# Kernel optimization log

Measured on AMD Instinct MI355X. Metric: run time of the kernel, lower is better.

The kernel has to match this reference:

```python
import jax, jax.numpy as jnp
import numpy as np

N_NODES = 400000
NUM_GRAPHS = 2048
IN_FEAT = 256
DENSE = 128
N_HEADS = 8


def setup_inputs() -> dict:
    key = jax.random.key(0)
    k_h, k_seg, k_w1, k_b1, k_w2, k_b2 = jax.random.split(key, 6)
    h = jax.random.normal(k_h, (N_NODES, IN_FEAT), dtype=jnp.float32)
    segment_ids = jnp.sort(
        jax.random.randint(k_seg, (N_NODES,), 0, NUM_GRAPHS, dtype=jnp.int32))
    # Linear params (jax convention: x @ W + b)
    W1 = jax.random.normal(k_w1, (IN_FEAT, DENSE), dtype=jnp.float32) / np.sqrt(IN_FEAT)
    b1 = jax.random.normal(k_b1, (DENSE,), dtype=jnp.float32) * 0.01
    W2 = jax.random.normal(k_w2, (DENSE, N_HEADS), dtype=jnp.float32) / np.sqrt(DENSE)
    b2 = jax.random.normal(k_b2, (N_HEADS,), dtype=jnp.float32) * 0.01
    return {"h": h, "segment_ids": segment_ids, "W1": W1, "b1": b1,
            "W2": W2, "b2": b2, "num_graphs": NUM_GRAPHS}


def reference(h, segment_ids, W1, b1, W2, b2, num_graphs):
    # scores: fc2(tanh(fc1(h))) -> [N, n_heads]
    scores = jnp.tanh(h @ W1 + b1) @ W2 + b2
    # ragged (per-graph) softmax over nodes, per head (dgl.softmax_nodes)
    seg_max = jax.ops.segment_max(scores, segment_ids, num_segments=num_graphs)  # [G, H]
    ex = jnp.exp(scores - seg_max[segment_ids])                                  # [N, H]
    denom = jax.ops.segment_sum(ex, segment_ids, num_segments=num_graphs)        # [G, H]
    attn = ex / denom[segment_ids]                                               # [N, H]
    # mean over heads of per-head weighted segment sums == segment sum with
    # head-averaged weights (linearity), avoiding H separate ndata passes.
    w = attn.mean(axis=1)                                                         # [N]
    out = jax.ops.segment_sum(h * w[:, None], segment_ids, num_segments=num_graphs)  # [G, in_feat]
    return out
```

## Files before the change

kernel.cpp:

```cpp
#include <hip/hip_runtime.h>
#include <hip/hip_bf16.h>

#define IN_FEAT 256
#define DENSE   128
#define NHEADS  8
#define MAXN    384
#define LDA     264
#define LDT     132
#define LDW2    132

typedef __attribute__((ext_vector_type(8))) short bf16x8_t;
typedef __attribute__((ext_vector_type(4))) float f32x4_t;

__device__ __forceinline__ unsigned int f2bf(float f) {
  unsigned int u = __float_as_uint(f);
  u += 0x7fffu + ((u >> 16) & 1u);
  return u >> 16;
}

__device__ __forceinline__ float fast_tanh(float x) {
  float ax = fabsf(x);
  float e = __expf(-2.0f * ax);
  float t = (1.0f - e) / (1.0f + e);
  return copysignf(t, x);
}

__global__ void seg_offsets_kernel(const int* __restrict__ seg, int* __restrict__ offs,
                                   int N, int G) {
  int i = blockIdx.x * blockDim.x + threadIdx.x;
  if (i >= N) return;
  int s  = seg[i];
  int sp = (i == 0) ? -1 : seg[i - 1];
  for (int g = sp + 1; g <= s; ++g) offs[g] = i;
  if (i == N - 1) {
    for (int g = s + 1; g <= G; ++g) offs[g] = N;
  }
}

__device__ __forceinline__ int lower_bound_dev(const int* __restrict__ seg, int N, int v) {
  int lo = 0, hi = N;
  while (lo < hi) {
    int mid = (lo + hi) >> 1;
    if (seg[mid] < v) lo = mid + 1; else hi = mid;
  }
  return lo;
}

__launch_bounds__(256, 3)
__global__ void attn_pool_kernel(const float* __restrict__ h,
                                 const int* __restrict__ seg,
                                 const int* __restrict__ offs,
                                 const float* __restrict__ W1,
                                 const float* __restrict__ b1,
                                 const float* __restrict__ W2,
                                 const float* __restrict__ b2,
                                 float* __restrict__ out,
                                 int N) {
  __shared__ short sA[64 * LDA];
  __shared__ float sScores[MAXN * NHEADS];
  __shared__ float sWgt[MAXN];
  __shared__ float sW2T[NHEADS * LDW2];
  __shared__ float sB1[DENSE];
  __shared__ float sB2[NHEADS];
  __shared__ float sRed[64];
  __shared__ float sMax[NHEADS];
  __shared__ float sInvD[NHEADS];

  const int g   = blockIdx.x;
  const int tid = threadIdx.x;

  int start, end;
  if (offs != nullptr) {
    start = offs[g];
    end   = offs[g + 1];
  } else {
    start = lower_bound_dev(seg, N, g);
    end   = lower_bound_dev(seg, N, g + 1);
  }
  int n = end - start;
  if (n > MAXN) n = MAXN;

  float* sT = (float*)sA;

  if (n == 0) {
    if (tid < IN_FEAT) out[(size_t)g * IN_FEAT + tid] = 0.0f;
    return;
  }

  for (int idx = tid; idx < DENSE * NHEADS; idx += 256) {
    int k = idx >> 3; int hd = idx & 7;
    sW2T[hd * LDW2 + k] = W2[idx];
  }
  if (tid < DENSE)  sB1[tid] = b1[tid];
  if (tid < NHEADS) sB2[tid] = b2[tid];

  const int lane = tid & 63;
  const int wv   = tid >> 6;
  const int lr   = lane & 15;
  const int q    = lane >> 4;

  bf16x8_t b1f[16];
  #pragma unroll
  for (int ct = 0; ct < 2; ++ct) {
    int colb = wv * 32 + ct * 16 + lr;
    #pragma unroll
    for (int ks = 0; ks < 8; ++ks) {
      bf16x8_t bb;
      #pragma unroll
      for (int j = 0; j < 8; ++j) {
        float f = W1[(ks * 32 + q * 8 + j) * DENSE + colb];
        bb[j] = (short)f2bf(f);
      }
      b1f[ct * 8 + ks] = bb;
    }
  }

  const int ntiles = (n + 63) >> 6;
  for (int t = 0; t < ntiles; ++t) {
    const int m0   = start + t * 64;
    const int rem  = n - t * 64;
    const int mcnt = rem < 64 ? rem : 64;
    __syncthreads();

    #pragma unroll
    for (int it = 0; it < 16; ++it) {
      int row = it * 4 + (tid >> 6);
      int f4  = tid & 63;
      float4 v = make_float4(0.f, 0.f, 0.f, 0.f);
      if (row < mcnt) v = *(const float4*)(h + (size_t)(m0 + row) * IN_FEAT + f4 * 4);
      unsigned int p0 = f2bf(v.x) | (f2bf(v.y) << 16);
      unsigned int p1 = f2bf(v.z) | (f2bf(v.w) << 16);
      *(uint2*)&sA[row * LDA + f4 * 4] = make_uint2(p0, p1);
    }
    __syncthreads();

    f32x4_t acc[4][2];
    #pragma unroll
    for (int mt = 0; mt < 4; ++mt) {
      acc[mt][0] = (f32x4_t){0, 0, 0, 0};
      acc[mt][1] = (f32x4_t){0, 0, 0, 0};
    }
    #pragma unroll
    for (int ks = 0; ks < 8; ++ks) {
      bf16x8_t a0 = *(const bf16x8_t*)&sA[( 0 + lr) * LDA + ks * 32 + q * 8];
      bf16x8_t a1 = *(const bf16x8_t*)&sA[(16 + lr) * LDA + ks * 32 + q * 8];
      bf16x8_t a2 = *(const bf16x8_t*)&sA[(32 + lr) * LDA + ks * 32 + q * 8];
      bf16x8_t a3 = *(const bf16x8_t*)&sA[(48 + lr) * LDA + ks * 32 + q * 8];
      acc[0][0] = __builtin_amdgcn_mfma_f32_16x16x32_bf16(a0, b1f[ks],     acc[0][0], 0, 0, 0);
      acc[0][1] = __builtin_amdgcn_mfma_f32_16x16x32_bf16(a0, b1f[8 + ks], acc[0][1], 0, 0, 0);
      acc[1][0] = __builtin_amdgcn_mfma_f32_16x16x32_bf16(a1, b1f[ks],     acc[1][0], 0, 0, 0);
      acc[1][1] = __builtin_amdgcn_mfma_f32_16x16x32_bf16(a1, b1f[8 + ks], acc[1][1], 0, 0, 0);
      acc[2][0] = __builtin_amdgcn_mfma_f32_16x16x32_bf16(a2, b1f[ks],     acc[2][0], 0, 0, 0);
      acc[2][1] = __builtin_amdgcn_mfma_f32_16x16x32_bf16(a2, b1f[8 + ks], acc[2][1], 0, 0, 0);
      acc[3][0] = __builtin_amdgcn_mfma_f32_16x16x32_bf16(a3, b1f[ks],     acc[3][0], 0, 0, 0);
      acc[3][1] = __builtin_amdgcn_mfma_f32_16x16x32_bf16(a3, b1f[8 + ks], acc[3][1], 0, 0, 0);
    }
    __syncthreads();

    #pragma unroll
    for (int mt = 0; mt < 4; ++mt) {
      int rbase = mt * 16 + q * 4;
      #pragma unroll
      for (int ct = 0; ct < 2; ++ct) {
        int col = wv * 32 + ct * 16 + lr;
        float bias = sB1[col];
        #pragma unroll
        for (int r = 0; r < 4; ++r)
          sT[(rbase + r) * LDT + col] = fast_tanh(acc[mt][ct][r] + bias);
      }
    }
    __syncthreads();

    {
      int i0 = tid >> 3;
      int hd = tid & 7;
      #pragma unroll
      for (int half = 0; half < 2; ++half) {
        int i = i0 + half * 32;
        if (i < mcnt) {
          float s = sB2[hd];
          #pragma unroll
          for (int k4 = 0; k4 < DENSE; k4 += 4) {
            float4 tv  = *(const float4*)&sT[i * LDT + k4];
            float4 wv2 = *(const float4*)&sW2T[hd * LDW2 + k4];
            s = fmaf(tv.x, wv2.x, s); s = fmaf(tv.y, wv2.y, s);
            s = fmaf(tv.z, wv2.z, s); s = fmaf(tv.w, wv2.w, s);
          }
          sScores[(t * 64 + i) * NHEADS + hd] = s;
        }
      }
    }
  }
  __syncthreads();

  if (tid < 64) {
    int hd = tid & 7, ch = tid >> 3;
    float m = -3.4e38f;
    for (int i = ch; i < n; i += 8) m = fmaxf(m, sScores[i * NHEADS + hd]);
    sRed[tid] = m;
  }
  __syncthreads();
  if (tid < NHEADS) {
    float m = sRed[tid];
    #pragma unroll
    for (int j = 1; j < 8; ++j) m = fmaxf(m, sRed[j * 8 + tid]);
    sMax[tid] = m;
  }
  __syncthreads();
  if (tid < 64) {
    int hd = tid & 7, ch = tid >> 3;
    float mm = sMax[hd], ssum = 0.f;
    for (int i = ch; i < n; i += 8) {
      float e = __expf(sScores[i * NHEADS + hd] - mm);
      sScores[i * NHEADS + hd] = e;
      ssum += e;
    }
    sRed[tid] = ssum;
  }
  __syncthreads();
  if (tid < NHEADS) {
    float d = 0.f;
    #pragma unroll
    for (int j = 0; j < 8; ++j) d += sRed[j * 8 + tid];
    sInvD[tid] = 1.0f / d;
  }
  __syncthreads();
  for (int i = tid; i < n; i += 256) {
    float w = 0.f;
    #pragma unroll
    for (int hd = 0; hd < NHEADS; ++hd) w += sScores[i * NHEADS + hd] * sInvD[hd];
    sWgt[i] = 0.125f * w;
  }
  __syncthreads();

  {
    int grp = tid >> 6;
    int c4  = lane << 2;
    float4 acc = make_float4(0.f, 0.f, 0.f, 0.f);
    for (int i = grp; i < n; i += 4) {
      float w = sWgt[i];
      float4 hv = *(const float4*)(h + (size_t)(start + i) * IN_FEAT + c4);
      acc.x = fmaf(w, hv.x, acc.x);
      acc.y = fmaf(w, hv.y, acc.y);
      acc.z = fmaf(w, hv.z, acc.z);
      acc.w = fmaf(w, hv.w, acc.w);
    }
    float* sPart = (float*)sA;
    *(float4*)&sPart[grp * IN_FEAT + c4] = acc;
    __syncthreads();
    {
      float o = 0.f;
      #pragma unroll
      for (int p = 0; p < 4; ++p) o += sPart[p * IN_FEAT + tid];
      out[(size_t)g * IN_FEAT + tid] = o;
    }
  }
}

extern "C" void kernel_launch(void* const* d_in, const int* in_sizes, int n_in,
                              void* d_out, int out_size, void* d_ws, size_t ws_size,
                              hipStream_t stream) {
  const float* h   = (const float*)d_in[0];
  const int*   seg = (const int*)d_in[1];
  const float* W1  = (const float*)d_in[2];
  const float* b1v = (const float*)d_in[3];
  const float* W2  = (const float*)d_in[4];
  const float* b2v = (const float*)d_in[5];
  float* out = (float*)d_out;
  const int N = in_sizes[0] / IN_FEAT;
  const int G = out_size / IN_FEAT;

  int* offs = nullptr;
  if (ws_size >= (size_t)(G + 1) * sizeof(int)) {
    offs = (int*)d_ws;
    seg_offsets_kernel<<<(N + 255) / 256, 256, 0, stream>>>(seg, offs, N, G);
  }
  attn_pool_kernel<<<G, 256, 0, stream>>>(h, seg, offs, W1, b1v, W2, b2v, out, N);
}
```

Measured before the change: 237.5 us.

## Prefetch next h tile into registers and prepack W1 bf16 fragments

Adds a small kernel that converts W1 once into bf16 MFMA fragment order in the workspace, so the main kernel reads packed fragments each k-step instead of holding 16 converted fragments in registers. The main kernel also software-pipelines the h tile load: the next 64-row tile is issued into registers while the current tile runs its MFMAs. Tanh is applied in registers before the LDS store, and the softmax reductions now use all 256 threads instead of 64. The aim is to hide global load latency and cut per-block W1 conversion, at the cost of 64 prefetch registers, repeated W1 fragment reads from cache every tile, and one extra launch.

```diff
diff --git a/kernel.cpp b/kernel.cpp
--- a/kernel.cpp
+++ b/kernel.cpp
@@ -37,6 +37,27 @@
   }
 }
 
+__global__ void w1_frag_kernel(const float* __restrict__ W1, unsigned int* __restrict__ w1f) {
+  int t = blockIdx.x * blockDim.x + threadIdx.x;
+  if (t >= 4096) return;
+  int lane = t & 63;
+  int fid  = t >> 6;
+  int ct = fid & 1;
+  int ks = (fid >> 1) & 7;
+  int wv = fid >> 4;
+  int col = wv * 32 + ct * 16 + (lane & 15);
+  int k0  = ks * 32 + (lane >> 4) * 8;
+  unsigned int p[4];
+  #pragma unroll
+  for (int jj = 0; jj < 4; ++jj) {
+    unsigned int lo = f2bf(W1[(size_t)(k0 + 2 * jj) * DENSE + col]);
+    unsigned int hi = f2bf(W1[(size_t)(k0 + 2 * jj + 1) * DENSE + col]);
+    p[jj] = lo | (hi << 16);
+  }
+  uint4 v = make_uint4(p[0], p[1], p[2], p[3]);
+  *(uint4*)&w1f[(size_t)t * 4] = v;
+}
+
 __device__ __forceinline__ int lower_bound_dev(const int* __restrict__ seg, int N, int v) {
   int lo = 0, hi = N;
   while (lo < hi) {
@@ -51,6 +72,7 @@
                                  const int* __restrict__ seg,
                                  const int* __restrict__ offs,
                                  const float* __restrict__ W1,
+                                 const unsigned int* __restrict__ w1f,
                                  const float* __restrict__ b1,
                                  const float* __restrict__ W2,
                                  const float* __restrict__ b2,
@@ -62,7 +84,7 @@
   __shared__ float sW2T[NHEADS * LDW2];
   __shared__ float sB1[DENSE];
   __shared__ float sB2[NHEADS];
-  __shared__ float sRed[64];
+  __shared__ float sRed[256];
   __shared__ float sMax[NHEADS];
   __shared__ float sInvD[NHEADS];
 
@@ -87,35 +109,32 @@
     return;
   }
 
-  for (int idx = tid; idx < DENSE * NHEADS; idx += 256) {
-    int k = idx >> 3; int hd = idx & 7;
-    sW2T[hd * LDW2 + k] = W2[idx];
-  }
-  if (tid < DENSE)  sB1[tid] = b1[tid];
-  if (tid < NHEADS) sB2[tid] = b2[tid];
-
   const int lane = tid & 63;
   const int wv   = tid >> 6;
   const int lr   = lane & 15;
   const int q    = lane >> 4;
-
-  bf16x8_t b1f[16];
-  #pragma unroll
-  for (int ct = 0; ct < 2; ++ct) {
-    int colb = wv * 32 + ct * 16 + lr;
-    #pragma unroll
-    for (int ks = 0; ks < 8; ++ks) {
-      bf16x8_t bb;
-      #pragma unroll
-      for (int j = 0; j < 8; ++j) {
-        float f = W1[(ks * 32 + q * 8 + j) * DENSE + colb];
-        bb[j] = (short)f2bf(f);
-      }
-      b1f[ct * 8 + ks] = bb;
-    }
-  }
-
   const int ntiles = (n + 63) >> 6;
+
+  float4 pf[16];
+  const int pfr  = tid >> 6;
+  const int pfc4 = (tid & 63) * 4;
+  auto pf_issue = [&](int m0_) {
+    #pragma unroll
+    for (int it = 0; it < 16; ++it) {
+      int rr = m0_ + it * 4 + pfr;
+      rr = (rr < end) ? rr : start;
+      pf[it] = *(const float4*)(h + (size_t)rr * IN_FEAT + pfc4);
+    }
+  };
+  pf_issue(start);
+
+  for (int idx = tid; idx < DENSE * NHEADS; idx += 256) {
+    int k = idx >> 3; int hd = idx & 7;
+    sW2T[hd * LDW2 + k] = W2[idx];
+  }
+  if (tid < DENSE)  sB1[tid] = b1[tid];
+  if (tid < NHEADS) sB2[tid] = b2[tid];
+
   for (int t = 0; t < ntiles; ++t) {
     const int m0   = start + t * 64;
     const int rem  = n - t * 64;
@@ -124,15 +143,16 @@
 
     #pragma unroll
     for (int it = 0; it < 16; ++it) {
-      int row = it * 4 + (tid >> 6);
-      int f4  = tid & 63;
-      float4 v = make_float4(0.f, 0.f, 0.f, 0.f);
-      if (row < mcnt) v = *(const float4*)(h + (size_t)(m0 + row) * IN_FEAT + f4 * 4);
+      int row = it * 4 + pfr;
+      float4 v = pf[it];
+      if (row >= mcnt) v = make_float4(0.f, 0.f, 0.f, 0.f);
       unsigned int p0 = f2bf(v.x) | (f2bf(v.y) << 16);
       unsigned int p1 = f2bf(v.z) | (f2bf(v.w) << 16);
-      *(uint2*)&sA[row * LDA + f4 * 4] = make_uint2(p0, p1);
-    }
-    __syncthreads();
+      *(uint2*)&sA[row * LDA + pfc4] = make_uint2(p0, p1);
+    }
+    __syncthreads();
+
+    if (t + 1 < ntiles) pf_issue(m0 + 64);
 
     f32x4_t acc[4][2];
     #pragma unroll
@@ -140,21 +160,56 @@
       acc[mt][0] = (f32x4_t){0, 0, 0, 0};
       acc[mt][1] = (f32x4_t){0, 0, 0, 0};
     }
-    #pragma unroll
-    for (int ks = 0; ks < 8; ++ks) {
-      bf16x8_t a0 = *(const bf16x8_t*)&sA[( 0 + lr) * LDA + ks * 32 + q * 8];
-      bf16x8_t a1 = *(const bf16x8_t*)&sA[(16 + lr) * LDA + ks * 32 + q * 8];
-      bf16x8_t a2 = *(const bf16x8_t*)&sA[(32 + lr) * LDA + ks * 32 + q * 8];
-      bf16x8_t a3 = *(const bf16x8_t*)&sA[(48 + lr) * LDA + ks * 32 + q * 8];
-      acc[0][0] = __builtin_amdgcn_mfma_f32_16x16x32_bf16(a0, b1f[ks],     acc[0][0], 0, 0, 0);
-      acc[0][1] = __builtin_amdgcn_mfma_f32_16x16x32_bf16(a0, b1f[8 + ks], acc[0][1], 0, 0, 0);
-      acc[1][0] = __builtin_amdgcn_mfma_f32_16x16x32_bf16(a1, b1f[ks],     acc[1][0], 0, 0, 0);
-      acc[1][1] = __builtin_amdgcn_mfma_f32_16x16x32_bf16(a1, b1f[8 + ks], acc[1][1], 0, 0, 0);
-      acc[2][0] = __builtin_amdgcn_mfma_f32_16x16x32_bf16(a2, b1f[ks],     acc[2][0], 0, 0, 0);
-      acc[2][1] = __builtin_amdgcn_mfma_f32_16x16x32_bf16(a2, b1f[8 + ks], acc[2][1], 0, 0, 0);
-      acc[3][0] = __builtin_amdgcn_mfma_f32_16x16x32_bf16(a3, b1f[ks],     acc[3][0], 0, 0, 0);
-      acc[3][1] = __builtin_amdgcn_mfma_f32_16x16x32_bf16(a3, b1f[8 + ks], acc[3][1], 0, 0, 0);
-    }
+
+#define FC1_KS(ks, WF0, WF1)                                                          \
+    {                                                                                 \
+      bf16x8_t a0 = *(const bf16x8_t*)&sA[( 0 + lr) * LDA + (ks) * 32 + q * 8];       \
+      bf16x8_t a1 = *(const bf16x8_t*)&sA[(16 + lr) * LDA + (ks) * 32 + q * 8];       \
+      bf16x8_t a2 = *(const bf16x8_t*)&sA[(32 + lr) * LDA + (ks) * 32 + q * 8];       \
+      bf16x8_t a3 = *(const bf16x8_t*)&sA[(48 + lr) * LDA + (ks) * 32 + q * 8];       \
+      acc[0][0] = __builtin_amdgcn_mfma_f32_16x16x32_bf16(a0, WF0, acc[0][0], 0, 0, 0); \
+      acc[0][1] = __builtin_amdgcn_mfma_f32_16x16x32_bf16(a0, WF1, acc[0][1], 0, 0, 0); \
+      acc[1][0] = __builtin_amdgcn_mfma_f32_16x16x32_bf16(a1, WF0, acc[1][0], 0, 0, 0); \
+      acc[1][1] = __builtin_amdgcn_mfma_f32_16x16x32_bf16(a1, WF1, acc[1][1], 0, 0, 0); \
+      acc[2][0] = __builtin_amdgcn_mfma_f32_16x16x32_bf16(a2, WF0, acc[2][0], 0, 0, 0); \
+      acc[2][1] = __builtin_amdgcn_mfma_f32_16x16x32_bf16(a2, WF1, acc[2][1], 0, 0, 0); \
+      acc[3][0] = __builtin_amdgcn_mfma_f32_16x16x32_bf16(a3, WF0, acc[3][0], 0, 0, 0); \
+      acc[3][1] = __builtin_amdgcn_mfma_f32_16x16x32_bf16(a3, WF1, acc[3][1], 0, 0, 0); \
+    }
+
+    if (w1f != nullptr) {
+      const bf16x8_t* w1fv = (const bf16x8_t*)w1f;
+      #pragma unroll
+      for (int ks = 0; ks < 8; ++ks) {
+        int f0 = ((wv * 8 + ks) * 2) * 64 + lane;
+        bf16x8_t wf0 = w1fv[f0];
+        bf16x8_t wf1 = w1fv[f0 + 64];
+        FC1_KS(ks, wf0, wf1)
+      }
+    } else {
+      #pragma unroll
+      for (int ks = 0; ks < 8; ++ks) {
+        bf16x8_t wf0, wf1;
+        #pragma unroll
+        for (int j = 0; j < 8; ++j) {
+          int k = ks * 32 + q * 8 + j;
+          wf0[j] = (short)f2bf(W1[(size_t)k * DENSE + wv * 32 + lr]);
+          wf1[j] = (short)f2bf(W1[(size_t)k * DENSE + wv * 32 + 16 + lr]);
+        }
+        FC1_KS(ks, wf0, wf1)
+      }
+    }
+#undef FC1_KS
+
+    #pragma unroll
+    for (int mt = 0; mt < 4; ++mt)
+      #pragma unroll
+      for (int ct = 0; ct < 2; ++ct) {
+        float bias = sB1[wv * 32 + ct * 16 + lr];
+        #pragma unroll
+        for (int r = 0; r < 4; ++r)
+          acc[mt][ct][r] = fast_tanh(acc[mt][ct][r] + bias);
+      }
     __syncthreads();
 
     #pragma unroll
@@ -163,10 +218,9 @@
       #pragma unroll
       for (int ct = 0; ct < 2; ++ct) {
         int col = wv * 32 + ct * 16 + lr;
-        float bias = sB1[col];
         #pragma unroll
         for (int r = 0; r < 4; ++r)
-          sT[(rbase + r) * LDT + col] = fast_tanh(acc[mt][ct][r] + bias);
+          sT[(rbase + r) * LDT + col] = acc[mt][ct][r];
       }
     }
     __syncthreads();
@@ -193,45 +247,42 @@
   }
   __syncthreads();
 
-  if (tid < 64) {
-    int hd = tid & 7, ch = tid >> 3;
+  {
+    const int hd = tid & 7, ch = tid >> 3;
     float m = -3.4e38f;
-    for (int i = ch; i < n; i += 8) m = fmaxf(m, sScores[i * NHEADS + hd]);
+    for (int i = ch; i < n; i += 32) m = fmaxf(m, sScores[i * NHEADS + hd]);
     sRed[tid] = m;
-  }
-  __syncthreads();
-  if (tid < NHEADS) {
-    float m = sRed[tid];
-    #pragma unroll
-    for (int j = 1; j < 8; ++j) m = fmaxf(m, sRed[j * 8 + tid]);
-    sMax[tid] = m;
-  }
-  __syncthreads();
-  if (tid < 64) {
-    int hd = tid & 7, ch = tid >> 3;
+    __syncthreads();
+    if (tid < NHEADS) {
+      float mm = sRed[tid];
+      #pragma unroll
+      for (int j = 1; j < 32; ++j) mm = fmaxf(mm, sRed[j * 8 + tid]);
+      sMax[tid] = mm;
+    }
+    __syncthreads();
     float mm = sMax[hd], ssum = 0.f;
-    for (int i = ch; i < n; i += 8) {
+    for (int i = ch; i < n; i += 32) {
       float e = __expf(sScores[i * NHEADS + hd] - mm);
       sScores[i * NHEADS + hd] = e;
       ssum += e;
     }
     sRed[tid] = ssum;
-  }
-  __syncthreads();
-  if (tid < NHEADS) {
-    float d = 0.f;
-    #pragma unroll
-    for (int j = 0; j < 8; ++j) d += sRed[j * 8 + tid];
-    sInvD[tid] = 1.0f / d;
-  }
-  __syncthreads();
-  for (int i = tid; i < n; i += 256) {
-    float w = 0.f;
-    #pragma unroll
-    for (int hd = 0; hd < NHEADS; ++hd) w += sScores[i * NHEADS + hd] * sInvD[hd];
-    sWgt[i] = 0.125f * w;
-  }
-  __syncthreads();
+    __syncthreads();
+    if (tid < NHEADS) {
+      float d = 0.f;
+      #pragma unroll
+      for (int j = 0; j < 32; ++j) d += sRed[j * 8 + tid];
+      sInvD[tid] = 1.0f / d;
+    }
+    __syncthreads();
+    for (int i = tid; i < n; i += 256) {
+      float w = 0.f;
+      #pragma unroll
+      for (int hd2 = 0; hd2 < NHEADS; ++hd2) w += sScores[i * NHEADS + hd2] * sInvD[hd2];
+      sWgt[i] = 0.125f * w;
+    }
+    __syncthreads();
+  }
 
   {
     int grp = tid >> 6;
@@ -270,10 +321,19 @@
   const int N = in_sizes[0] / IN_FEAT;
   const int G = out_size / IN_FEAT;
 
+  const size_t offs_bytes = (size_t)(G + 1) * sizeof(int);
+  const size_t w1f_off    = (offs_bytes + 255) & ~(size_t)255;
+  const size_t w1f_bytes  = 4096 * 16;
+
   int* offs = nullptr;
-  if (ws_size >= (size_t)(G + 1) * sizeof(int)) {
+  unsigned int* w1f = nullptr;
+  if (ws_size >= offs_bytes) {
     offs = (int*)d_ws;
     seg_offsets_kernel<<<(N + 255) / 256, 256, 0, stream>>>(seg, offs, N, G);
   }
-  attn_pool_kernel<<<G, 256, 0, stream>>>(h, seg, offs, W1, b1v, W2, b2v, out, N);
-}
+  if (ws_size >= w1f_off + w1f_bytes) {
+    w1f = (unsigned int*)((char*)d_ws + w1f_off);
+    w1_frag_kernel<<<16, 256, 0, stream>>>(W1, w1f);
+  }
+  attn_pool_kernel<<<G, 256, 0, stream>>>(h, seg, offs, W1, w1f, b1v, W2, b2v, out, N);
+}
```

After: 307.5 us. 1.29x slower.
